# Kernel optimization log

Hardware: AMD Instinct MI355X
Metric: run time of the kernel (lower is better)

Reference implementation:

```python
import jax, jax.numpy as jnp
import numpy as np

B, N, C = 4, 2048, 1024
H = 16
D = C // H  # 64
EMB = 1024
EPS = 1e-5


def _ln(x):
    # LayerNorm over last dim, no affine (FiLM / per-head norm supplies scale/shift)
    mu = jnp.mean(x, axis=-1, keepdims=True)
    var = jnp.var(x, axis=-1, keepdims=True)
    return (x - mu) * jax.lax.rsqrt(var + EPS)


def setup_inputs() -> dict:
    key = jax.random.key(0)
    ks = jax.random.split(key, 6)
    x = jax.random.normal(ks[0], (B, N, C), dtype=jnp.float32)
    emb = jax.random.normal(ks[1], (B, N, EMB), dtype=jnp.float32)
    # emb_layer: Linear(emb_dim, 2*dim)
    W_emb = jax.random.normal(ks[2], (2 * C, EMB), dtype=jnp.float32) * (1.0 / np.sqrt(EMB))
    b_emb = jnp.zeros((2 * C,), dtype=jnp.float32)
    # proj: Linear(dim, 3*dim, bias=False)
    W_proj = jax.random.normal(ks[3], (3 * C, C), dtype=jnp.float32) * (1.0 / np.sqrt(C))
    # out: Linear(dim, dim, bias=False); zero-init in source, random here for a meaningful baseline
    W_out = jax.random.normal(ks[4], (C, C), dtype=jnp.float32) * (1.0 / np.sqrt(C))
    return {"x": x, "emb": emb, "W_emb": W_emb, "b_emb": b_emb,
            "W_proj": W_proj, "W_out": W_out}


def reference(x, emb, W_emb, b_emb, W_proj, W_out):
    # FiLM-conditioned norm
    se = emb @ W_emb.T + b_emb                      # (B,N,2C)
    scale, shift = jnp.split(se, 2, axis=-1)
    h = _ln(x) * (1.0 + scale) + shift              # (B,N,C)
    # QKV projection + split into heads: 'b n (qkv h d) -> qkv b h n d'
    qkv = (h @ W_proj.T).reshape(B, N, 3, H, D).transpose(2, 0, 3, 1, 4)
    q, k, v = qkv[0], qkv[1], qkv[2]                # each (B,H,N,D)
    # per-head q/k normalization (Normalize over dim_head)
    q = _ln(q)
    k = _ln(k)
    # scaled dot-product attention
    attn = jax.nn.softmax(jnp.einsum('bhnd,bhmd->bhnm', q, k) * (1.0 / np.sqrt(D)), axis=-1)
    o = jnp.einsum('bhnm,bhmd->bhnd', attn, v)      # (B,H,N,D)
    o = o.transpose(0, 2, 1, 3).reshape(B, N, C)    # 'b h n d -> b n (h d)'
    return o + o @ W_out.T
```

## Files before the change

### kernel.cpp

```cpp
#include <hip/hip_runtime.h>

#define B_ 4
#define N_ 2048
#define C_ 1024
#define H_ 16
#define D_ 64
#define ROWS (B_ * N_)

typedef __bf16 bf16x8 __attribute__((ext_vector_type(8)));
typedef float f32x4 __attribute__((ext_vector_type(4)));
typedef unsigned short ushort_t;

__device__ inline float b2f(ushort_t u) {
    union { unsigned int i; float f; } v; v.i = ((unsigned int)u) << 16; return v.f;
}
__device__ inline ushort_t f2b(float f) {
    union { float f; unsigned int i; } v; v.f = f;
    unsigned int r = v.i + 0x7fffu + ((v.i >> 16) & 1u);
    return (ushort_t)(r >> 16);
}

__device__ inline bool detect_f32(const ushort_t* u) {
    int huge = 0;
#pragma unroll
    for (int i = 0; i < 64; ++i) {
        int ex = (u[2 * i] >> 7) & 0xFF;
        huge |= (ex >= 0xC0) ? 1 : 0;
    }
    return huge != 0;
}

__global__ __launch_bounds__(256) void cvt_bf16(
    const void* __restrict__ src, ushort_t* __restrict__ dst, int n_elts)
{
    const bool s32 = detect_f32((const ushort_t*)src);
    const int start = (blockIdx.x * 256 + threadIdx.x) * 8;
    const int stride = gridDim.x * 256 * 8;
    if (s32) {
        const float* s = (const float*)src;
        for (int i = start; i < n_elts; i += stride) {
            float4 a = *(const float4*)(s + i);
            float4 b = *(const float4*)(s + i + 4);
            ushort4 w0, w1;
            w0.x = f2b(a.x); w0.y = f2b(a.y); w0.z = f2b(a.z); w0.w = f2b(a.w);
            w1.x = f2b(b.x); w1.y = f2b(b.y); w1.z = f2b(b.z); w1.w = f2b(b.w);
            *(ushort4*)(dst + i)     = w0;
            *(ushort4*)(dst + i + 4) = w1;
        }
    } else {
        const ushort_t* s = (const ushort_t*)src;
        for (int i = start; i < n_elts; i += stride)
            *(uint4*)(dst + i) = *(const uint4*)(s + i);
    }
}

template<bool HAS_BIAS, bool HAS_RES, bool A_EXT, bool B_EXT, bool OUT_DYN, bool LN_QK>
__global__ __launch_bounds__(256) void gemm_bt(
    const void* __restrict__ A,
    const void* __restrict__ Bm,
    const ushort_t* __restrict__ bias,
    const ushort_t* __restrict__ resid,
    void* __restrict__ Cc,
    int M, int N, int K,
    const ushort_t* e0, const ushort_t* e1, const ushort_t* e2,
    const ushort_t* e3, const ushort_t* e4)
{
    const bool a32 = A_EXT ? detect_f32((const ushort_t*)A)  : false;
    const bool b32 = B_EXT ? detect_f32((const ushort_t*)Bm) : false;
    bool out32 = false;
    if constexpr (OUT_DYN)
        out32 = detect_f32(e0) && detect_f32(e1) && detect_f32(e2) &&
                detect_f32(e3) && detect_f32(e4);

    __shared__ __align__(16) ushort_t As[128][32];
    __shared__ __align__(16) ushort_t Bs[128][32];
    const int tid  = threadIdx.x;
    const int wave = tid >> 6, lane = tid & 63;
    const int lo = lane & 15, hi = lane >> 4;
    const int bm = blockIdx.x * 128, bn = blockIdx.y * 128;
    const int wm = (wave & 1) * 64,  wn = (wave >> 1) * 64;

    f32x4 acc[4][4] = {};

    for (int k0 = 0; k0 < K; k0 += 32) {
        if (a32) {
            const float* Af = (const float*)A;
#pragma unroll
            for (int i = 0; i < 4; ++i) {
                int c = tid + i * 256;
                int r = c >> 3, c4 = (c & 7) * 4;
                float4 v = *(const float4*)(Af + (size_t)(bm + r) * K + k0 + c4);
                ushort4 w; w.x = f2b(v.x); w.y = f2b(v.y); w.z = f2b(v.z); w.w = f2b(v.w);
                *(ushort4*)(&As[r][c4]) = w;
            }
        } else {
            const ushort_t* Ab = (const ushort_t*)A;
#pragma unroll
            for (int i = 0; i < 2; ++i) {
                int c = tid + i * 256;
                int r = c >> 2, c8 = (c & 3) * 8;
                *(uint4*)(&As[r][c8]) = *(const uint4*)(Ab + (size_t)(bm + r) * K + k0 + c8);
            }
        }
        if (b32) {
            const float* Bf = (const float*)Bm;
#pragma unroll
            for (int i = 0; i < 4; ++i) {
                int c = tid + i * 256;
                int r = c >> 3, c4 = (c & 7) * 4;
                float4 v = *(const float4*)(Bf + (size_t)(bn + r) * K + k0 + c4);
                ushort4 w; w.x = f2b(v.x); w.y = f2b(v.y); w.z = f2b(v.z); w.w = f2b(v.w);
                *(ushort4*)(&Bs[r][c4]) = w;
            }
        } else {
            const ushort_t* Bb = (const ushort_t*)Bm;
#pragma unroll
            for (int i = 0; i < 2; ++i) {
                int c = tid + i * 256;
                int r = c >> 2, c8 = (c & 3) * 8;
                *(uint4*)(&Bs[r][c8]) = *(const uint4*)(Bb + (size_t)(bn + r) * K + k0 + c8);
            }
        }
        __syncthreads();

        bf16x8 af[4], bfr[4];
#pragma unroll
        for (int i = 0; i < 4; ++i) af[i]  = *(const bf16x8*)(&As[wm + i * 16 + lo][hi * 8]);
#pragma unroll
        for (int j = 0; j < 4; ++j) bfr[j] = *(const bf16x8*)(&Bs[wn + j * 16 + lo][hi * 8]);
#pragma unroll
        for (int i = 0; i < 4; ++i)
#pragma unroll
            for (int j = 0; j < 4; ++j)
                acc[i][j] = __builtin_amdgcn_mfma_f32_16x16x32_bf16(af[i], bfr[j], acc[i][j], 0, 0, 0);
        __syncthreads();
    }

    if constexpr (LN_QK) {
        if (bn + wn < 2 * C_) {
#pragma unroll
            for (int i = 0; i < 4; ++i) {
#pragma unroll
                for (int r = 0; r < 4; ++r) {
                    float s = 0.0f, sq = 0.0f;
#pragma unroll
                    for (int j = 0; j < 4; ++j) {
                        float v = acc[i][j][r];
                        s += v; sq += v * v;
                    }
#pragma unroll
                    for (int off = 1; off < 16; off <<= 1) {
                        s  += __shfl_xor(s, off, 16);
                        sq += __shfl_xor(sq, off, 16);
                    }
                    const float mu   = s * (1.0f / 64.0f);
                    const float var  = sq * (1.0f / 64.0f) - mu * mu;
                    const float rstd = rsqrtf(var + 1e-5f);
#pragma unroll
                    for (int j = 0; j < 4; ++j)
                        acc[i][j][r] = (acc[i][j][r] - mu) * rstd;
                }
            }
        }
    }

#pragma unroll
    for (int i = 0; i < 4; ++i) {
#pragma unroll
        for (int j = 0; j < 4; ++j) {
            const int n = bn + wn + j * 16 + lo;
            float bv = HAS_BIAS ? b2f(bias[n]) : 0.0f;
#pragma unroll
            for (int r = 0; r < 4; ++r) {
                const int m = bm + wm + i * 16 + hi * 4 + r;
                float v = acc[i][j][r] + bv;
                if (HAS_RES) v += b2f(resid[(size_t)m * N + n]);
                if (OUT_DYN && out32) ((float*)Cc)[(size_t)m * N + n] = v;
                else                  ((ushort_t*)Cc)[(size_t)m * N + n] = f2b(v);
            }
        }
    }
}

__global__ __launch_bounds__(256) void ln_film(
    const void* __restrict__ x,
    const ushort_t* __restrict__ se,
    ushort_t* __restrict__ h)
{
    const bool x32 = detect_f32((const ushort_t*)x);
    const int row = blockIdx.x;
    const int t = threadIdx.x;
    const int wave = t >> 6, lane = t & 63;

    float f0, f1, f2, f3;
    if (x32) {
        float4 v = *(const float4*)((const float*)x + (size_t)row * C_ + t * 4);
        f0 = v.x; f1 = v.y; f2 = v.z; f3 = v.w;
    } else {
        ushort4 v = *(const ushort4*)((const ushort_t*)x + (size_t)row * C_ + t * 4);
        f0 = b2f(v.x); f1 = b2f(v.y); f2 = b2f(v.z); f3 = b2f(v.w);
    }
    float s  = f0 + f1 + f2 + f3;
    float sq = f0 * f0 + f1 * f1 + f2 * f2 + f3 * f3;
#pragma unroll
    for (int off = 32; off >= 1; off >>= 1) {
        s  += __shfl_xor(s, off);
        sq += __shfl_xor(sq, off);
    }
    __shared__ float red[8];
    if (lane == 0) { red[wave] = s; red[4 + wave] = sq; }
    __syncthreads();
    s  = red[0] + red[1] + red[2] + red[3];
    sq = red[4] + red[5] + red[6] + red[7];
    const float mu   = s * (1.0f / C_);
    const float var  = sq * (1.0f / C_) - mu * mu;
    const float rstd = rsqrtf(var + 1e-5f);

    const ushort_t* ser = se + (size_t)row * (2 * C_);
    ushort4 sc = *(const ushort4*)(ser + t * 4);
    ushort4 sh = *(const ushort4*)(ser + C_ + t * 4);
    ushort4 out;
    out.x = f2b((f0 - mu) * rstd * (1.0f + b2f(sc.x)) + b2f(sh.x));
    out.y = f2b((f1 - mu) * rstd * (1.0f + b2f(sc.y)) + b2f(sh.y));
    out.z = f2b((f2 - mu) * rstd * (1.0f + b2f(sc.z)) + b2f(sh.z));
    out.w = f2b((f3 - mu) * rstd * (1.0f + b2f(sc.w)) + b2f(sh.w));
    *(ushort4*)(h + (size_t)row * C_ + t * 4) = out;
}

__global__ __launch_bounds__(256) void vtrans(
    const ushort_t* __restrict__ qkv,
    ushort_t* __restrict__ vT)
{
    const int bh = blockIdx.x, b = bh >> 4, hh = bh & 15;
    const int n0 = blockIdx.y * 64;
    const int t = threadIdx.x;
    __shared__ ushort_t Vs[64][65];

    const int r = t >> 2, c0 = (t & 3) * 16;
    const ushort_t* src = qkv + (size_t)(b * N_ + n0 + r) * (3 * C_) + 2 * C_ + hh * D_;
#pragma unroll
    for (int i = 0; i < 16; ++i) Vs[r][c0 + i] = src[c0 + i];
    __syncthreads();
    const int d = t >> 2, j0 = (t & 3) * 16;
    ushort_t* dst = vT + ((size_t)bh * D_ + d) * N_ + n0;
#pragma unroll
    for (int i = 0; i < 16; ++i) dst[j0 + i] = Vs[j0 + i][d];
}

__global__ __launch_bounds__(512) void flash_attn(
    const ushort_t* __restrict__ qkv,
    const ushort_t* __restrict__ vT,
    ushort_t* __restrict__ o)
{
    const int bh = blockIdx.x, b = bh >> 4, hh = bh & 15;
    const int qb = blockIdx.y;
    const int tid = threadIdx.x;
    const int wave = tid >> 6, lane = tid & 63;
    const int lo = lane & 15, hi = lane >> 4;

    __shared__ __align__(16) ushort_t Ks[2][64 * 64];
    __shared__ __align__(16) ushort_t Vsh[2][64 * 64];
    __shared__ __align__(16) ushort_t Pl[8][16][72];

    const int sr = tid >> 3, sc = tid & 7;
    const int lsw = sr * 64 + ((sc ^ (sr & 7)) * 8);

    const int qrow = qb * 128 + wave * 16;
    const ushort_t* qp = qkv + (size_t)(b * N_ + qrow + lo) * (3 * C_) + hh * D_;
    const bf16x8 a0 = *(const bf16x8*)(qp + hi * 8);
    const bf16x8 a1 = *(const bf16x8*)(qp + 32 + hi * 8);

    const ushort_t* Kg = qkv + (size_t)b * N_ * (3 * C_) + C_ + hh * D_;
    const ushort_t* Vg = vT + (size_t)bh * D_ * N_;

    f32x4 accO[4] = {};
    float m_r[4], l_r[4];
#pragma unroll
    for (int r = 0; r < 4; ++r) { m_r[r] = -1e30f; l_r[r] = 0.0f; }
    const f32x4 zero = {0.f, 0.f, 0.f, 0.f};
    const float SC = 0.125f * 1.44269504f;

    const int q0 = (hi ^ (lo & 7)) * 8;
    const int q1 = ((4 + hi) ^ (lo & 7)) * 8;

    uint4 kst, vst;
    kst = *(const uint4*)(Kg + (size_t)sr * (3 * C_) + sc * 8);
    vst = *(const uint4*)(Vg + (size_t)sr * N_ + sc * 8);
    *(uint4*)(&Ks[0][lsw])  = kst;
    *(uint4*)(&Vsh[0][lsw]) = vst;
    __syncthreads();
    int cur = 0;

    for (int kt = 0; kt < N_; kt += 64) {
        const bool more = (kt + 64 < N_);
        if (more) {
            kst = *(const uint4*)(Kg + (size_t)(kt + 64 + sr) * (3 * C_) + sc * 8);
            vst = *(const uint4*)(Vg + (size_t)sr * N_ + (kt + 64) + sc * 8);
        }
        __builtin_amdgcn_sched_barrier(0);

        const ushort_t* Kc = &Ks[cur][0];
        f32x4 S[4];
#pragma unroll
        for (int g = 0; g < 4; ++g) {
            const int R = g * 16 + lo;
            bf16x8 kl = *(const bf16x8*)(Kc + R * 64 + q0);
            bf16x8 kh = *(const bf16x8*)(Kc + R * 64 + q1);
            f32x4 s0 = __builtin_amdgcn_mfma_f32_16x16x32_bf16(a0, kl, zero, 0, 0, 0);
            S[g]     = __builtin_amdgcn_mfma_f32_16x16x32_bf16(a1, kh, s0,   0, 0, 0);
        }

        float sv[4][4], pmax[4];
#pragma unroll
        for (int r = 0; r < 4; ++r) {
            float s0 = S[0][r] * SC, s1 = S[1][r] * SC;
            float s2 = S[2][r] * SC, s3 = S[3][r] * SC;
            sv[r][0] = s0; sv[r][1] = s1; sv[r][2] = s2; sv[r][3] = s3;
            float mx = fmaxf(fmaxf(s0, s1), fmaxf(s2, s3));
#pragma unroll
            for (int off = 1; off < 16; off <<= 1) mx = fmaxf(mx, __shfl_xor(mx, off, 16));
            pmax[r] = mx;
        }
        int needi = 0;
#pragma unroll
        for (int r = 0; r < 4; ++r) needi |= (pmax[r] > m_r[r] + 11.0f) ? 1 : 0;
        if (__any(needi)) {
#pragma unroll
            for (int r = 0; r < 4; ++r) {
                float mnew  = fmaxf(m_r[r], pmax[r]);
                float alpha = __builtin_amdgcn_exp2f(m_r[r] - mnew);
                m_r[r] = mnew;
                l_r[r] *= alpha;
#pragma unroll
                for (int ds = 0; ds < 4; ++ds) accO[ds][r] *= alpha;
            }
        }
#pragma unroll
        for (int r = 0; r < 4; ++r) {
            float rs = 0.0f;
#pragma unroll
            for (int g = 0; g < 4; ++g) {
                float pv = __builtin_amdgcn_exp2f(sv[r][g] - m_r[r]);
                Pl[wave][hi * 4 + r][g * 16 + lo] = f2b(pv);
                rs += pv;
            }
#pragma unroll
            for (int off = 1; off < 16; off <<= 1) rs += __shfl_xor(rs, off, 16);
            l_r[r] += rs;
        }

        asm volatile("s_waitcnt lgkmcnt(0)" ::: "memory");
        __builtin_amdgcn_sched_barrier(0);

        bf16x8 pf0 = *(const bf16x8*)(&Pl[wave][lo][hi * 8]);
        bf16x8 pf1 = *(const bf16x8*)(&Pl[wave][lo][32 + hi * 8]);
        const ushort_t* Vc = &Vsh[cur][0];
#pragma unroll
        for (int ds = 0; ds < 4; ++ds) {
            const int R = ds * 16 + lo;
            bf16x8 vf0 = *(const bf16x8*)(Vc + R * 64 + q0);
            bf16x8 vf1 = *(const bf16x8*)(Vc + R * 64 + q1);
            accO[ds] = __builtin_amdgcn_mfma_f32_16x16x32_bf16(pf0, vf0, accO[ds], 0, 0, 0);
            accO[ds] = __builtin_amdgcn_mfma_f32_16x16x32_bf16(pf1, vf1, accO[ds], 0, 0, 0);
        }

        if (more) {
            *(uint4*)(&Ks[cur ^ 1][lsw])  = kst;
            *(uint4*)(&Vsh[cur ^ 1][lsw]) = vst;
            __syncthreads();
            cur ^= 1;
        }
    }

#pragma unroll
    for (int ds = 0; ds < 4; ++ds)
#pragma unroll
        for (int r = 0; r < 4; ++r) {
            const int row = qrow + hi * 4 + r;
            float val = accO[ds][r] / l_r[r];
            o[((size_t)(b * N_ + row)) * C_ + hh * D_ + ds * 16 + lo] = f2b(val);
        }
}

__global__ __launch_bounds__(256) void attn_simple(
    const ushort_t* __restrict__ qkv,
    ushort_t* __restrict__ o)
{
    const int bh = blockIdx.x, b = bh >> 4, hh = bh & 15;
    const int t = threadIdx.x, lane = t & 63, wave = t >> 6;
    __shared__ float sc[N_];
    __shared__ float qrow[D_];
    __shared__ float red[4];
    __shared__ float opart[4][D_];

    const size_t hbase = (size_t)b * N_ * (3 * C_) + (size_t)hh * D_;

    for (int qi = 0; qi < 128; ++qi) {
        const int qr = blockIdx.y * 128 + qi;
        if (t < 64) qrow[t] = b2f(qkv[hbase + (size_t)qr * (3 * C_) + t]);
        __syncthreads();

        float myS[8];
        float mymax = -1e30f;
#pragma unroll
        for (int jj = 0; jj < 8; ++jj) {
            const int j = t + jj * 256;
            const bf16x8* kr = (const bf16x8*)(qkv + hbase + (size_t)j * (3 * C_) + C_);
            float s = 0.0f;
#pragma unroll
            for (int c = 0; c < 8; ++c) {
                bf16x8 kv = kr[c];
#pragma unroll
                for (int e = 0; e < 8; ++e) s += qrow[c * 8 + e] * (float)kv[e];
            }
            s *= 0.125f;
            myS[jj] = s;
            mymax = fmaxf(mymax, s);
        }
#pragma unroll
        for (int off = 32; off >= 1; off >>= 1) mymax = fmaxf(mymax, __shfl_xor(mymax, off));
        if (lane == 0) red[wave] = mymax;
        __syncthreads();
        const float M = fmaxf(fmaxf(red[0], red[1]), fmaxf(red[2], red[3]));

        float mysum = 0.0f;
#pragma unroll
        for (int jj = 0; jj < 8; ++jj) {
            float p = __expf(myS[jj] - M);
            sc[t + jj * 256] = p;
            mysum += p;
        }
#pragma unroll
        for (int off = 32; off >= 1; off >>= 1) mysum += __shfl_xor(mysum, off);
        __syncthreads();
        if (lane == 0) red[wave] = mysum;
        __syncthreads();
        const float L = red[0] + red[1] + red[2] + red[3];

        float acc = 0.0f;
        const int d = lane;
        const ushort_t* vb = qkv + hbase + 2 * C_ + d;
        for (int j = wave * 512; j < wave * 512 + 512; ++j)
            acc += sc[j] * b2f(vb[(size_t)j * (3 * C_)]);
        opart[wave][d] = acc;
        __syncthreads();
        if (t < 64) {
            float val = (opart[0][t] + opart[1][t] + opart[2][t] + opart[3][t]) / L;
            o[((size_t)(b * N_ + qr)) * C_ + hh * D_ + t] = f2b(val);
        }
        __syncthreads();
    }
}

extern "C" void kernel_launch(void* const* d_in, const int* in_sizes, int n_in,
                              void* d_out, int out_size, void* d_ws, size_t ws_size,
                              hipStream_t stream)
{
    const void* x = nullptr; const void* emb = nullptr;
    const void* W_emb = nullptr; const void* b_emb = nullptr;
    const void* W_proj = nullptr; const void* W_out = nullptr;
    int big_seen = 0;
    for (int i = 0; i < n_in; ++i) {
        const int s = in_sizes[i];
        if      (s == ROWS * C_)   { if (big_seen++ == 0) x = d_in[i]; else emb = d_in[i]; }
        else if (s == 2 * C_ * C_) W_emb  = d_in[i];
        else if (s == 3 * C_ * C_) W_proj = d_in[i];
        else if (s == C_ * C_)     W_out  = d_in[i];
        else if (s == 2 * C_)      b_emb  = d_in[i];
    }

    char* ws = (char*)d_ws;
    const size_t MB = 1024 * 1024;
    ushort_t* h       = (ushort_t*)(ws);
    ushort_t* se      = (ushort_t*)(ws + 16 * MB);
    ushort_t* qkv     = (ushort_t*)(ws + 16 * MB);
    ushort_t* o       = (ushort_t*)(ws);
    ushort_t* vT      = (ushort_t*)(ws + 64 * MB);
    ushort_t* wemb_bf = (ushort_t*)(ws + 48 * MB);
    ushort_t* emb_bf  = (ushort_t*)(ws + 58 * MB);
    ushort_t* wprj_bf = (ushort_t*)(ws + 74 * MB);
    const bool use_flash = (ws_size >= 80 * MB);

    const ushort_t* e0 = (const ushort_t*)x;
    const ushort_t* e1 = (const ushort_t*)emb;
    const ushort_t* e2 = (const ushort_t*)W_emb;
    const ushort_t* e3 = (const ushort_t*)W_proj;
    const ushort_t* e4 = (const ushort_t*)W_out;

    cvt_bf16<<<2048, 256, 0, stream>>>(emb,    emb_bf,  ROWS * C_);
    cvt_bf16<<<1024, 256, 0, stream>>>(W_emb,  wemb_bf, 2 * C_ * C_);
    cvt_bf16<<<1024, 256, 0, stream>>>(W_proj, wprj_bf, 3 * C_ * C_);

    gemm_bt<true, false, false, false, false, false><<<dim3(ROWS / 128, 2048 / 128), 256, 0, stream>>>(
        emb_bf, wemb_bf, (const ushort_t*)b_emb, nullptr, se, ROWS, 2048, 1024,
        e0, e1, e2, e3, e4);
    ln_film<<<ROWS, 256, 0, stream>>>(x, se, h);
    gemm_bt<false, false, false, false, false, true><<<dim3(ROWS / 128, 3072 / 128), 256, 0, stream>>>(
        h, wprj_bf, nullptr, nullptr, qkv, ROWS, 3072, 1024,
        e0, e1, e2, e3, e4);
    if (use_flash) {
        vtrans<<<dim3(B_ * H_, N_ / 64), 256, 0, stream>>>(qkv, vT);
        flash_attn<<<dim3(B_ * H_, N_ / 128), 512, 0, stream>>>(qkv, vT, o);
    } else {
        attn_simple<<<dim3(B_ * H_, N_ / 128), 256, 0, stream>>>(qkv, o);
    }
    gemm_bt<false, true, false, true, true, false><<<dim3(ROWS / 128, 1024 / 128), 256, 0, stream>>>(
        o, W_out, nullptr, o, d_out, ROWS, 1024, 1024,
        e0, e1, e2, e3, e4);
}
```

Measured before the change: 558.7 us.

## Swizzle GEMM tiles per XCD and double flash-attention query rows per block

Remaps GEMM workgroup IDs so consecutive tiles land on the same XCD, improving L2 locality of shared A/B panels. Flash attention now uses 1024-thread blocks covering 256 query rows, with half the threads staging K and the other half V, halving redundant K/V tile loads per query. The larger blocks reduce grid size and may limit scheduling flexibility or occupancy.

Result: slower. 596.9 us (+6.8%).

```diff
diff --git a/kernel.cpp b/kernel.cpp
--- a/kernel.cpp
+++ b/kernel.cpp
@@ -77,7 +77,14 @@
     const int tid  = threadIdx.x;
     const int wave = tid >> 6, lane = tid & 63;
     const int lo = lane & 15, hi = lane >> 4;
-    const int bm = blockIdx.x * 128, bn = blockIdx.y * 128;
+
+    const int nwg = gridDim.x * gridDim.y;
+    const int w   = blockIdx.y * gridDim.x + blockIdx.x;
+    const int cpx = nwg >> 3;
+    const int wp  = (w & 7) * cpx + (w >> 3);
+    const int bx  = wp % gridDim.x, by = wp / gridDim.x;
+
+    const int bm = bx * 128, bn = by * 128;
     const int wm = (wave & 1) * 64,  wn = (wave >> 1) * 64;
 
     f32x4 acc[4][4] = {};
@@ -90,8 +97,8 @@
                 int c = tid + i * 256;
                 int r = c >> 3, c4 = (c & 7) * 4;
                 float4 v = *(const float4*)(Af + (size_t)(bm + r) * K + k0 + c4);
-                ushort4 w; w.x = f2b(v.x); w.y = f2b(v.y); w.z = f2b(v.z); w.w = f2b(v.w);
-                *(ushort4*)(&As[r][c4]) = w;
+                ushort4 w4; w4.x = f2b(v.x); w4.y = f2b(v.y); w4.z = f2b(v.z); w4.w = f2b(v.w);
+                *(ushort4*)(&As[r][c4]) = w4;
             }
         } else {
             const ushort_t* Ab = (const ushort_t*)A;
@@ -109,8 +116,8 @@
                 int c = tid + i * 256;
                 int r = c >> 3, c4 = (c & 7) * 4;
                 float4 v = *(const float4*)(Bf + (size_t)(bn + r) * K + k0 + c4);
-                ushort4 w; w.x = f2b(v.x); w.y = f2b(v.y); w.z = f2b(v.z); w.w = f2b(v.w);
-                *(ushort4*)(&Bs[r][c4]) = w;
+                ushort4 w4; w4.x = f2b(v.x); w4.y = f2b(v.y); w4.z = f2b(v.z); w4.w = f2b(v.w);
+                *(ushort4*)(&Bs[r][c4]) = w4;
             }
         } else {
             const ushort_t* Bb = (const ushort_t*)Bm;
@@ -247,7 +254,7 @@
     for (int i = 0; i < 16; ++i) dst[j0 + i] = Vs[j0 + i][d];
 }
 
-__global__ __launch_bounds__(512) void flash_attn(
+__global__ __launch_bounds__(1024) void flash_attn(
     const ushort_t* __restrict__ qkv,
     const ushort_t* __restrict__ vT,
     ushort_t* __restrict__ o)
@@ -260,12 +267,14 @@
 
     __shared__ __align__(16) ushort_t Ks[2][64 * 64];
     __shared__ __align__(16) ushort_t Vsh[2][64 * 64];
-    __shared__ __align__(16) ushort_t Pl[8][16][72];
-
-    const int sr = tid >> 3, sc = tid & 7;
+    __shared__ __align__(16) ushort_t Pl[16][16][72];
+
+    const bool isK = tid < 512;
+    const int st = tid & 511;
+    const int sr = st >> 3, sc = st & 7;
     const int lsw = sr * 64 + ((sc ^ (sr & 7)) * 8);
 
-    const int qrow = qb * 128 + wave * 16;
+    const int qrow = qb * 256 + wave * 16;
     const ushort_t* qp = qkv + (size_t)(b * N_ + qrow + lo) * (3 * C_) + hh * D_;
     const bf16x8 a0 = *(const bf16x8*)(qp + hi * 8);
     const bf16x8 a1 = *(const bf16x8*)(qp + 32 + hi * 8);
@@ -283,19 +292,22 @@
     const int q0 = (hi ^ (lo & 7)) * 8;
     const int q1 = ((4 + hi) ^ (lo & 7)) * 8;
 
-    uint4 kst, vst;
-    kst = *(const uint4*)(Kg + (size_t)sr * (3 * C_) + sc * 8);
-    vst = *(const uint4*)(Vg + (size_t)sr * N_ + sc * 8);
-    *(uint4*)(&Ks[0][lsw])  = kst;
-    *(uint4*)(&Vsh[0][lsw]) = vst;
+    uint4 stg;
+    if (isK) {
+        stg = *(const uint4*)(Kg + (size_t)sr * (3 * C_) + sc * 8);
+        *(uint4*)(&Ks[0][lsw]) = stg;
+    } else {
+        stg = *(const uint4*)(Vg + (size_t)sr * N_ + sc * 8);
+        *(uint4*)(&Vsh[0][lsw]) = stg;
+    }
     __syncthreads();
     int cur = 0;
 
     for (int kt = 0; kt < N_; kt += 64) {
         const bool more = (kt + 64 < N_);
         if (more) {
-            kst = *(const uint4*)(Kg + (size_t)(kt + 64 + sr) * (3 * C_) + sc * 8);
-            vst = *(const uint4*)(Vg + (size_t)sr * N_ + (kt + 64) + sc * 8);
+            if (isK) stg = *(const uint4*)(Kg + (size_t)(kt + 64 + sr) * (3 * C_) + sc * 8);
+            else     stg = *(const uint4*)(Vg + (size_t)sr * N_ + (kt + 64) + sc * 8);
         }
         __builtin_amdgcn_sched_barrier(0);
 
@@ -365,8 +377,8 @@
         }
 
         if (more) {
-            *(uint4*)(&Ks[cur ^ 1][lsw])  = kst;
-            *(uint4*)(&Vsh[cur ^ 1][lsw]) = vst;
+            if (isK) *(uint4*)(&Ks[cur ^ 1][lsw]) = stg;
+            else     *(uint4*)(&Vsh[cur ^ 1][lsw]) = stg;
             __syncthreads();
             cur ^= 1;
         }
@@ -500,7 +512,7 @@
         e0, e1, e2, e3, e4);
     if (use_flash) {
         vtrans<<<dim3(B_ * H_, N_ / 64), 256, 0, stream>>>(qkv, vT);
-        flash_attn<<<dim3(B_ * H_, N_ / 128), 512, 0, stream>>>(qkv, vT, o);
+        flash_attn<<<dim3(B_ * H_, N_ / 256), 1024, 0, stream>>>(qkv, vT, o);
     } else {
         attn_simple<<<dim3(B_ * H_, N_ / 128), 256, 0, stream>>>(qkv, o);
     }
```
